# Optimization experiments

Measured on AMD Instinct MI355X. Metric: run time of the kernel, lower is better.

The kernel has to match this reference:

```python
import jax, jax.numpy as jnp
import numpy as np

H = 8
BLEN = 256
NEG = -1e9

def _mask2d(blen, h=32, win=6):
    # precomputed 2D-local mask for tail blocks: query pos in [blen, 2blen),
    # key pos in [0, 2blen); causal + Chebyshev-ish window on a width-h image grid
    cp = np.arange(blen, 2 * blen)[:, None]
    op = np.arange(2 * blen)[None, :]
    causal = op <= cp
    ch, cw = cp // h, cp % h
    oh, ow = op // h, op % h
    ok = causal & (np.abs(ch - oh) <= win) & (np.abs(cw - ow) <= win)
    return np.where(ok, 0.0, NEG).astype(np.float32)

def _causal_mask(blen):
    return np.where(np.tril(np.ones((blen, blen), bool)), 0.0, NEG).astype(np.float32)

def _attn(X, Wq, Wk, Wv, Wo):
    B, L, D = X.shape
    dh = D // H
    split = lambda Y: Y.reshape(B, L, H, dh).transpose(0, 2, 1, 3)  # [B,H,L,dh]
    q = split(X @ Wq) * (dh ** -0.5)
    k = split(X @ Wk)
    v = split(X @ Wv)
    pad = (-L) % BLEN
    if pad:
        q, k, v = (jnp.pad(t, ((0, 0), (0, 0), (0, pad), (0, 0))) for t in (q, k, v))
    Lp = L + pad
    n = Lp // BLEN
    bias1 = jnp.asarray(_causal_mask(BLEN))
    logits1 = jnp.einsum('bhqd,bhkd->bhqk', q[:, :, :BLEN], k[:, :, :BLEN]) + bias1
    first = jax.nn.softmax(logits1, axis=-1) @ v[:, :, :BLEN]  # [B,H,BLEN,dh]
    if n > 1:
        qb = q.reshape(B, H, n, BLEN, dh)
        kb = k.reshape(B, H, n, BLEN, dh)
        vb = v.reshape(B, H, n, BLEN, dh)
        local_k = jnp.concatenate([kb[:, :, :-1], kb[:, :, 1:]], axis=3)  # [B,H,n-1,2B,dh]
        local_v = jnp.concatenate([vb[:, :, :-1], vb[:, :, 1:]], axis=3)
        bias2 = jnp.asarray(_mask2d(BLEN))
        logits2 = jnp.einsum('bhnqd,bhnkd->bhnqk', qb[:, :, 1:], local_k) + bias2
        tail = jnp.einsum('bhnqk,bhnkd->bhnqd', jax.nn.softmax(logits2, axis=-1), local_v)
        tail = tail.reshape(B, H, (n - 1) * BLEN, dh)
        res = jnp.concatenate([first, tail], axis=2)[:, :, :L]
    else:
        res = first[:, :, :L]
    res = res.transpose(0, 2, 1, 3).reshape(B, L, D)
    return res @ Wo

def _ln(x, g, b, eps=1e-6):
    m = x.mean(-1, keepdims=True)
    v = ((x - m) ** 2).mean(-1, keepdims=True)
    return (x - m) / jnp.sqrt(v + eps) * g + b

def setup_inputs() -> dict:
    key = jax.random.key(0)
    ks = jax.random.split(key, 8)
    D, F = 256, 512
    s = 0.02
    return {
        'X': jax.random.normal(ks[0], (32, 1024, D), jnp.float32),
        'Wq': jax.random.normal(ks[1], (D, D), jnp.float32) * s,
        'Wk': jax.random.normal(ks[2], (D, D), jnp.float32) * s,
        'Wv': jax.random.normal(ks[3], (D, D), jnp.float32) * s,
        'Wo': jax.random.normal(ks[4], (D, D), jnp.float32) * s,
        'ln1_g': jnp.ones((D,), jnp.float32),
        'ln1_b': jnp.zeros((D,), jnp.float32),
        'W1': jax.random.normal(ks[5], (D, F), jnp.float32) * s,
        'b1': jnp.zeros((F,), jnp.float32),
        'W2': jax.random.normal(ks[6], (F, D), jnp.float32) * s,
        'b2': jnp.zeros((D,), jnp.float32),
        'ln2_g': jnp.ones((D,), jnp.float32),
        'ln2_b': jnp.zeros((D,), jnp.float32),
    }

def reference(X, Wq, Wk, Wv, Wo, ln1_g, ln1_b, W1, b1, W2, b2, ln2_g, ln2_b):
    y = _attn(X, Wq, Wk, Wv, Wo)
    X = _ln(y + X, ln1_g, ln1_b)
    y = jax.nn.relu(X @ W1 + b1) @ W2 + b2
    return _ln(y + X, ln2_g, ln2_b)
```

## Files before the change

kernel.cpp:

```cpp
#include <hip/hip_runtime.h>

typedef unsigned short u16;
typedef __attribute__((ext_vector_type(8))) short bh8;
typedef __attribute__((ext_vector_type(4))) short s4;
typedef __attribute__((ext_vector_type(4))) short bh4;
typedef __attribute__((ext_vector_type(4))) float fx4;

__device__ __forceinline__ u16 f2b(float f) {
  union { float f; unsigned u; } v; v.f = f;
  unsigned r = v.u + 0x7fffu + ((v.u >> 16) & 1u);
  return (u16)(r >> 16);
}
__device__ __forceinline__ float b2f(u16 h) {
  union { unsigned u; float f; } v; v.u = ((unsigned)h) << 16; return v.f;
}

__device__ __forceinline__ float ex2(float x) {
#if __has_builtin(__builtin_amdgcn_exp2f)
  return __builtin_amdgcn_exp2f(x);
#else
  return __expf(x * 0.6931471805599453f);
#endif
}

__device__ __forceinline__ unsigned cvtpk(float lo, float hi) {
  unsigned r;
  asm("v_cvt_pk_bf16_f32 %0, %1, %2" : "=v"(r) : "v"(lo), "v"(hi));
  return r;
}

#if __has_builtin(__builtin_amdgcn_mfma_f32_16x16x16bf16_1k)
__device__ __forceinline__ fx4 pv_mfma(s4 a, s4 b, fx4 c) {
  return __builtin_amdgcn_mfma_f32_16x16x16bf16_1k(a, b, c, 0, 0, 0);
}
#else
__device__ __forceinline__ fx4 pv_mfma(s4 a, s4 b, fx4 c) {
  asm("v_mfma_f32_16x16x16_bf16 %0, %1, %2, %0" : "+v"(c) : "v"(a), "v"(b));
  return c;
}
#endif

__global__ __launch_bounds__(256) void conv_w_k(const float* __restrict__ Wq, const float* __restrict__ Wk,
                         const float* __restrict__ Wv, const float* __restrict__ Wo,
                         const float* __restrict__ W1, const float* __restrict__ W2,
                         u16* __restrict__ WqkvT, u16* __restrict__ WoT,
                         u16* __restrict__ W1T, u16* __restrict__ W2T) {
  int i = blockIdx.x * 256 + threadIdx.x;
  if (i < 196608) {
    int n = i >> 8, k = i & 255; float v;
    if (n < 256) v = Wq[k*256+n] * 0.25503487359f;
    else if (n < 512) v = Wk[k*256+(n-256)];
    else v = Wv[k*256+(n-512)];
    WqkvT[i] = f2b(v);
  } else if (i < 262144) {
    int j = i - 196608; int n = j >> 8, k = j & 255;
    WoT[j] = f2b(Wo[k*256+n]);
  } else if (i < 393216) {
    int j = i - 262144; int n = j >> 8, k = j & 255;
    W1T[j] = f2b(W1[k*512+n]);
  } else {
    int j = i - 393216; int n = j >> 9, k = j & 511;
    W2T[j] = f2b(W2[k*256+n]);
  }
}

template<int K, int N, int EPI, int AF32>
__global__ __launch_bounds__(256) void gemm_k(
    const void* __restrict__ Av, const u16* __restrict__ BT,
    u16* __restrict__ C0, u16* __restrict__ C1, u16* __restrict__ C2,
    const float* __restrict__ bias) {
  constexpr int BK = 32;
  __shared__ u16 smem[AF32 ? 24576 : 16384];
  constexpr int ABUF = AF32 ? 8192 : 4096;
  constexpr int BOFF = AF32 ? 16384 : 8192;
  const int nx = gridDim.x;
  const int lid = blockIdx.y * nx + blockIdx.x;
  const int xcd = lid & 7;
  const int jj2 = lid >> 3;
  const int m0 = (xcd * (gridDim.y >> 3) + jj2 / nx) * 128;
  const int n0 = (jj2 % nx) * 128;
  const int tid = threadIdx.x, lane = tid & 63, wv = tid >> 6;
  const int wr = wv >> 1, wc = wv & 1, lg = lane >> 4, ll = lane & 15;
  const u16* A16 = (const u16*)Av;
  const float* A32 = (const float*)Av;

  fx4 acc[4][4] = {};

  auto stageB = [&](int buf, int ks) {
#pragma unroll
    for (int i = 0; i < 2; ++i) {
      int c = i*256 + tid;
      int row = c >> 2, ko = (c & 3) * 8;
      const u16* gpB = BT + (size_t)(n0+row)*K + ks + ko;
      int lbase = BOFF + buf*4096 + (i*256 + wv*64) * 8;
      __builtin_amdgcn_global_load_lds((const __attribute__((address_space(1))) void*)gpB,
          (__attribute__((address_space(3))) void*)&smem[lbase], 16, 0, 0);
    }
  };
  auto stageA16 = [&](int buf, int ks) {
#pragma unroll
    for (int i = 0; i < 2; ++i) {
      int c = i*256 + tid;
      int row = c >> 2, ko = (c & 3) * 8;
      const u16* gpA = A16 + (size_t)(m0+row)*K + ks + ko;
      int lbase = buf*ABUF + (i*256 + wv*64) * 8;
      __builtin_amdgcn_global_load_lds((const __attribute__((address_space(1))) void*)gpA,
          (__attribute__((address_space(3))) void*)&smem[lbase], 16, 0, 0);
    }
  };
  auto stageA32 = [&](int buf, int ks) {
#pragma unroll
    for (int i = 0; i < 4; ++i) {
      int c = i*256 + tid;
      int r = c >> 3;
      int po = (c & 7) * 16;
      int lo = po ^ ((r & 7) << 4);
      const float* gpA = A32 + (size_t)(m0 + r)*K + ks + (lo >> 2);
      int lbase = buf*ABUF + (i*256 + wv*64) * 8;
      __builtin_amdgcn_global_load_lds((const __attribute__((address_space(1))) void*)gpA,
          (__attribute__((address_space(3))) void*)&smem[lbase], 16, 0, 0);
    }
  };

  constexpr int NT = K / BK;
  if constexpr (AF32) stageA32(0, 0); else stageA16(0, 0);
  stageB(0, 0);
  __syncthreads();
  int cur = 0;
  for (int t = 0; t < NT; ++t) {
    if (t + 1 < NT) {
      if constexpr (AF32) stageA32(cur ^ 1, (t+1)*BK); else stageA16(cur ^ 1, (t+1)*BK);
      stageB(cur ^ 1, (t+1)*BK);
    }
    bh8 af[4], bfr[4];
    if constexpr (AF32) {
#pragma unroll
      for (int mi = 0; mi < 4; ++mi) {
        int r = wr*64 + mi*16 + ll;
        int sw = (r & 7) << 4;
        int b0 = r*128 + ((lg*32) ^ sw);
        int b1 = r*128 + ((lg*32 + 16) ^ sw);
        float4 a0 = *(const float4*)&smem[cur*ABUF + (b0 >> 1)];
        float4 a1 = *(const float4*)&smem[cur*ABUF + (b1 >> 1)];
        union { unsigned u[4]; bh8 v; } cvt;
        cvt.u[0] = cvtpk(a0.x, a0.y); cvt.u[1] = cvtpk(a0.z, a0.w);
        cvt.u[2] = cvtpk(a1.x, a1.y); cvt.u[3] = cvtpk(a1.z, a1.w);
        af[mi] = cvt.v;
      }
    } else {
#pragma unroll
      for (int mi = 0; mi < 4; ++mi)
        af[mi] = *(const bh8*)&smem[cur*ABUF + (wr*64 + mi*16 + ll)*BK + lg*8];
    }
#pragma unroll
    for (int ni = 0; ni < 4; ++ni)
      bfr[ni] = *(const bh8*)&smem[BOFF + cur*4096 + (wc*64 + ni*16 + ll)*BK + lg*8];
#pragma unroll
    for (int mi = 0; mi < 4; ++mi)
#pragma unroll
      for (int ni = 0; ni < 4; ++ni)
        acc[mi][ni] = __builtin_amdgcn_mfma_f32_16x16x32_bf16(af[mi], bfr[ni], acc[mi][ni], 0, 0, 0);
    __syncthreads();
    cur ^= 1;
  }

  auto swz = [](int r) { return ((r & 14) << 2) ^ ((r & 3) << 5); };
  const bool vt = (EPI == 0) && (n0 >= 512);

  if (!vt) {
    float bv[4];
    if constexpr (EPI >= 2) {
#pragma unroll
      for (int ni = 0; ni < 4; ++ni) bv[ni] = bias[n0 + wc*64 + ni*16 + ll];
    }
#pragma unroll
    for (int mi = 0; mi < 4; ++mi)
#pragma unroll
      for (int ni = 0; ni < 4; ++ni) {
        fx4 v = acc[mi][ni];
        int n = wc*64 + ni*16 + ll;
#pragma unroll
        for (int ii = 0; ii < 2; ++ii) {
          float x0 = v[2*ii], x1 = v[2*ii+1];
          if constexpr (EPI == 2) { x0 = fmaxf(x0 + bv[ni], 0.f); x1 = fmaxf(x1 + bv[ni], 0.f); }
          unsigned pk = cvtpk(x0, x1);
          int mA = wr*64 + mi*16 + lg*4 + 2*ii;
          int mB = mA + 1;
          smem[mA*128 + (n ^ swz(mA))] = (u16)pk;
          smem[mB*128 + (n ^ swz(mB))] = (u16)(pk >> 16);
        }
      }
  } else {
#pragma unroll
    for (int mi = 0; mi < 4; ++mi)
#pragma unroll
      for (int ni = 0; ni < 4; ++ni) {
        fx4 v = acc[mi][ni];
        int n = wc*64 + ni*16 + ll;
        int mb = wr*64 + mi*16 + lg*4;
        uint2 pk;
        pk.x = cvtpk(v[0], v[1]);
        pk.y = cvtpk(v[2], v[3]);
        *(uint2*)&smem[n*128 + (mb ^ swz(n))] = pk;
      }
  }
  __syncthreads();

#pragma unroll
  for (int j = 0; j < 8; ++j) {
    int cid = tid + 256*j;
    int row = cid >> 4, c8 = (cid & 15) << 3;
    bh8 val = *(const bh8*)&smem[row*128 + (c8 ^ swz(row))];
    if constexpr (EPI == 0) {
      if (!vt) {
        int m = m0 + row; int b = m >> 10, l = m & 1023;
        int n = n0 + c8; int hh = (n >> 5) & 7, d = n & 31;
        size_t bh_ = (size_t)(b*8 + hh);
        u16* dst = (n0 < 256) ? C0 : C1;
        *(bh8*)&dst[(bh_*1024 + l)*32 + d] = val;
      } else {
        int n = n0 + row; int hh = (n >> 5) & 7, d = n & 31;
        int m = m0 + c8; int b = m >> 10, l = m & 1023;
        size_t bh_ = (size_t)(b*8 + hh);
        *(bh8*)&C2[(bh_*32 + d)*1024 + l] = val;
      }
    } else {
      *(bh8*)&C0[(size_t)(m0+row)*N + n0 + c8] = val;
    }
  }
}

template<int K, int RF32, int OF32, int BIAS>
__global__ __launch_bounds__(256) void gemm_ln_k(
    const u16* __restrict__ A, const u16* __restrict__ BT,
    const void* __restrict__ resid, const float* __restrict__ bias,
    const float* __restrict__ g, const float* __restrict__ b,
    void* __restrict__ out) {
  constexpr int BK = 32;
  __shared__ u16 smem[20480];
  const int lid = blockIdx.y;
  const int xcd = lid & 7;
  const int jj2 = lid >> 3;
  const int m0 = (xcd * (gridDim.y >> 3) + jj2) * 64;
  const int tid = threadIdx.x, lane = tid & 63, wv = tid >> 6;
  const int wr = wv >> 1, wc = wv & 1, lg = lane >> 4, ll = lane & 15;

  fx4 acc[2][8] = {};

  auto stage = [&](int buf, int ks) {
    {
      int c = tid;
      int row = c >> 2, ko = (c & 3) * 8;
      const u16* gpA = A + (size_t)(m0+row)*K + ks + ko;
      int lbase = wv*512;
      __builtin_amdgcn_global_load_lds((const __attribute__((address_space(1))) void*)gpA,
          (__attribute__((address_space(3))) void*)&smem[buf*2048 + lbase], 16, 0, 0);
    }
#pragma unroll
    for (int i = 0; i < 4; ++i) {
      int c = i*256 + tid;
      int row = c >> 2, ko = (c & 3) * 8;
      const u16* gpB = BT + (size_t)row*K + ks + ko;
      int lbase = (i*256 + wv*64) * 8;
      __builtin_amdgcn_global_load_lds((const __attribute__((address_space(1))) void*)gpB,
          (__attribute__((address_space(3))) void*)&smem[4096 + buf*8192 + lbase], 16, 0, 0);
    }
  };

  constexpr int NT = K / BK;
  stage(0, 0);
  __syncthreads();
  int cur = 0;
  for (int t = 0; t < NT; ++t) {
    if (t + 1 < NT) stage(cur ^ 1, (t+1)*BK);
    bh8 af[2], bfr[8];
#pragma unroll
    for (int mi = 0; mi < 2; ++mi)
      af[mi] = *(const bh8*)&smem[cur*2048 + (wr*32 + mi*16 + ll)*BK + lg*8];
#pragma unroll
    for (int ni = 0; ni < 8; ++ni)
      bfr[ni] = *(const bh8*)&smem[4096 + cur*8192 + (wc*128 + ni*16 + ll)*BK + lg*8];
#pragma unroll
    for (int mi = 0; mi < 2; ++mi)
#pragma unroll
      for (int ni = 0; ni < 8; ++ni)
        acc[mi][ni] = __builtin_amdgcn_mfma_f32_16x16x32_bf16(bfr[ni], af[mi], acc[mi][ni], 0, 0, 0);
    __syncthreads();
    cur ^= 1;
  }

#pragma unroll
  for (int mi = 0; mi < 2; ++mi) {
    int m_l = wr*32 + mi*16 + ll;
    int sx = (m_l & 7) << 1;
#pragma unroll
    for (int ni = 0; ni < 8; ++ni) {
      fx4 v = acc[mi][ni];
      int gidx = (wc*32 + ni*4 + lg) ^ sx;
      uint2 pk;
      pk.x = cvtpk(v[0], v[1]);
      pk.y = cvtpk(v[2], v[3]);
      *(uint2*)&smem[m_l*256 + gidx*4] = pk;
    }
  }
  __syncthreads();

  const int c0 = lane * 4;
  float4 gv = *(const float4*)&g[c0];
  float4 bv = *(const float4*)&b[c0];
  float4 biasv = {0.f, 0.f, 0.f, 0.f};
  if constexpr (BIAS) biasv = *(const float4*)&bias[c0];
#pragma unroll 4
  for (int rr = 0; rr < 16; ++rr) {
    int r = wv*16 + rr;
    bh4 yv = *(const bh4*)&smem[r*256 + ((lane ^ ((r & 7) << 1)) << 2)];
    size_t gbase = (size_t)(m0 + r) * 256 + c0;
    float s0, s1, s2, s3;
    if constexpr (RF32) {
      float4 xv = *(const float4*)&((const float*)resid)[gbase];
      s0 = b2f((u16)yv[0]) + biasv.x + xv.x;
      s1 = b2f((u16)yv[1]) + biasv.y + xv.y;
      s2 = b2f((u16)yv[2]) + biasv.z + xv.z;
      s3 = b2f((u16)yv[3]) + biasv.w + xv.w;
    } else {
      bh4 xv = *(const bh4*)&((const u16*)resid)[gbase];
      s0 = b2f((u16)yv[0]) + biasv.x + b2f((u16)xv[0]);
      s1 = b2f((u16)yv[1]) + biasv.y + b2f((u16)xv[1]);
      s2 = b2f((u16)yv[2]) + biasv.z + b2f((u16)xv[2]);
      s3 = b2f((u16)yv[3]) + biasv.w + b2f((u16)xv[3]);
    }
    float sum = s0 + s1 + s2 + s3;
    float sq  = s0*s0 + s1*s1 + s2*s2 + s3*s3;
#pragma unroll
    for (int msk = 1; msk <= 32; msk <<= 1) {
      sum += __shfl_xor(sum, msk);
      sq  += __shfl_xor(sq, msk);
    }
    float mean = sum * 0.00390625f;
    float var  = sq  * 0.00390625f - mean*mean;
    float rs = rsqrtf(var + 1e-6f);
    float o0 = (s0 - mean)*rs*gv.x + bv.x;
    float o1 = (s1 - mean)*rs*gv.y + bv.y;
    float o2 = (s2 - mean)*rs*gv.z + bv.z;
    float o3 = (s3 - mean)*rs*gv.w + bv.w;
    if constexpr (OF32) {
      float4 o = {o0, o1, o2, o3};
      *(float4*)&((float*)out)[gbase] = o;
    } else {
      bh4 o;
      o[0] = (short)f2b(o0); o[1] = (short)f2b(o1);
      o[2] = (short)f2b(o2); o[3] = (short)f2b(o3);
      *(bh4*)&((u16*)out)[gbase] = o;
    }
  }
}

__global__ __launch_bounds__(256) void attn_k(
    const u16* __restrict__ qw, const u16* __restrict__ kw,
    const u16* __restrict__ vtw, u16* __restrict__ ao) {
  const int qb = blockIdx.x, hh = blockIdx.y, b = blockIdx.z;
  const int tid = threadIdx.x, lane = tid & 63, wv = tid >> 6;
  const int lg = lane >> 4, ll = lane & 15;
  const int kstart = qb ? (qb - 1) * 256 : 0;
  const size_t bh_ = (size_t)(b*8 + hh);
  const u16* kg = kw  + (bh_*1024 + kstart)*32;
  const u16* vg = vtw + bh_*32*1024 + kstart;
  const u16* qg = qw  + (bh_*1024 + qb*256)*32;

  bh8 qf[4];
#pragma unroll
  for (int qi = 0; qi < 4; ++qi)
    qf[qi] = *(const bh8*)&qg[(size_t)(wv*64 + qi*16 + ll)*32 + lg*8];

  fx4 oacc[4][2] = {};
  float lsum[4] = {0.f, 0.f, 0.f, 0.f};
  const fx4 zero = {0.f, 0.f, 0.f, 0.f};

  const int ch0 = wv*2;
  const int lo_w = qb ? ch0 + 2 : 0;
  const int hi_w = qb ? ch0 + 9 : ch0 + 1;

  for (int ohm = lo_w; ohm <= hi_w; ++ohm) {
    const int kb = ohm * 32;
    bh8 kf0 = *(const bh8*)&kg[(size_t)(kb + ll)*32 + lg*8];
    bh8 kf1 = *(const bh8*)&kg[(size_t)(kb + 16 + ll)*32 + lg*8];
    s4 vb[2][2];
#pragma unroll
    for (int cs = 0; cs < 2; ++cs)
#pragma unroll
      for (int dsub = 0; dsub < 2; ++dsub)
        vb[cs][dsub] = *(const s4*)&vg[(size_t)(dsub*16 + ll)*1024 + kb + cs*16 + lg*4];

#pragma unroll
    for (int qi = 0; qi < 4; ++qi) {
      const int ch = ch0 + (qi >> 1);
      const int dlo = qb ? ch + 2 : 0;
      const int dhi = qb ? ch + 8 : ch;
      if (ohm < dlo || ohm > dhi) continue;
      const bool diag = (ohm == dhi);

      fx4 s0 = __builtin_amdgcn_mfma_f32_16x16x32_bf16(kf0, qf[qi], zero, 0, 0, 0);
      fx4 s1 = __builtin_amdgcn_mfma_f32_16x16x32_bf16(kf1, qf[qi], zero, 0, 0, 0);

      const int cw = ll + ((qi & 1) << 4);
      float p[2][4];
      if (!qb && !diag) {
#pragma unroll
        for (int i = 0; i < 4; ++i) { p[0][i] = ex2(s0[i]); p[1][i] = ex2(s1[i]); }
      } else {
        const int off = (qb && !diag) ? 6 : 0;
        const unsigned thr = diag ? (qb ? 7u : 32u) : 13u;
#pragma unroll
        for (int cs = 0; cs < 2; ++cs) {
          const int tb = cw + off - cs*16 - lg*4;
          fx4 sv = cs ? s1 : s0;
#pragma unroll
          for (int i = 0; i < 4; ++i) {
            bool ok = (unsigned)(tb - i) < thr;
            p[cs][i] = ok ? ex2(sv[i]) : 0.f;
          }
        }
      }
      lsum[qi] += (p[0][0]+p[0][1]+p[0][2]+p[0][3]) + (p[1][0]+p[1][1]+p[1][2]+p[1][3]);

#pragma unroll
      for (int cs = 0; cs < 2; ++cs) {
        union { unsigned u[2]; s4 s; } cv;
        cv.u[0] = cvtpk(p[cs][0], p[cs][1]);
        cv.u[1] = cvtpk(p[cs][2], p[cs][3]);
#pragma unroll
        for (int dsub = 0; dsub < 2; ++dsub)
          oacc[qi][dsub] = pv_mfma(cv.s, vb[cs][dsub], oacc[qi][dsub]);
      }
    }
  }

  float rinv[4];
#pragma unroll
  for (int qi = 0; qi < 4; ++qi) {
    float v = lsum[qi];
    v += __shfl_xor(v, 16);
    v += __shfl_xor(v, 32);
    rinv[qi] = 1.0f / v;
  }

  u16* aop = ao + ((size_t)(b*1024 + qb*256))*256 + hh*32;
#pragma unroll
  for (int qi = 0; qi < 4; ++qi) {
    float rq[4];
#pragma unroll
    for (int i = 0; i < 4; ++i) rq[i] = __shfl(rinv[qi], lg*4 + i);
#pragma unroll
    for (int dsub = 0; dsub < 2; ++dsub)
#pragma unroll
      for (int i = 0; i < 4; ++i) {
        int q = wv*64 + qi*16 + lg*4 + i;
        aop[(size_t)q*256 + dsub*16 + ll] = f2b(oacc[qi][dsub][i] * rq[i]);
      }
  }
}

extern "C" void kernel_launch(void* const* d_in, const int* in_sizes, int n_in,
                              void* d_out, int out_size, void* d_ws, size_t ws_size,
                              hipStream_t stream) {
  const float* X    = (const float*)d_in[0];
  const float* Wq   = (const float*)d_in[1];
  const float* Wk   = (const float*)d_in[2];
  const float* Wv   = (const float*)d_in[3];
  const float* Wo   = (const float*)d_in[4];
  const float* ln1g = (const float*)d_in[5];
  const float* ln1b = (const float*)d_in[6];
  const float* W1   = (const float*)d_in[7];
  const float* b1   = (const float*)d_in[8];
  const float* W2   = (const float*)d_in[9];
  const float* b2   = (const float*)d_in[10];
  const float* ln2g = (const float*)d_in[11];
  const float* ln2b = (const float*)d_in[12];
  float* out = (float*)d_out;

  char* ws = (char*)d_ws;
  const size_t A = 32768ull * 256 * 2;
  u16* qws = (u16*)(ws + A);
  u16* kws = (u16*)(ws + 2*A);
  u16* vtw = (u16*)(ws + 3*A);
  u16* ao  = (u16*)(ws);
  u16* x1b = kws;
  u16* hw  = (u16*)(ws);
  u16* WqkvT = (u16*)(ws + 4*A);
  u16* WoT = WqkvT + 196608;
  u16* W1T = WoT + 65536;
  u16* W2T = W1T + 131072;

  conv_w_k<<<2048, 256, 0, stream>>>(Wq, Wk, Wv, Wo, W1, W2, WqkvT, WoT, W1T, W2T);
  gemm_k<256, 768, 0, 1><<<dim3(6, 256), 256, 0, stream>>>(X, WqkvT, qws, kws, vtw, nullptr);
  attn_k<<<dim3(4, 8, 32), 256, 0, stream>>>(qws, kws, vtw, ao);
  gemm_ln_k<256, 1, 0, 0><<<dim3(1, 512), 256, 0, stream>>>(ao, WoT, X, nullptr, ln1g, ln1b, x1b);
  gemm_k<256, 512, 2, 0><<<dim3(4, 256), 256, 0, stream>>>(x1b, W1T, hw, nullptr, nullptr, b1);
  gemm_ln_k<512, 0, 1, 1><<<dim3(1, 512), 256, 0, stream>>>(hw, W2T, x1b, b2, ln2g, ln2b, out);
}
```

Baseline: 119.6 us.

## Triple-buffer GEMM LDS staging with explicit vmcnt waits and raw barriers

```diff
diff --git a/kernel.cpp b/kernel.cpp
--- a/kernel.cpp
+++ b/kernel.cpp
@@ -39,6 +39,12 @@
   return c;
 }
 #endif
+
+#define SBAR() do { \
+  __builtin_amdgcn_sched_barrier(0); \
+  __builtin_amdgcn_s_barrier(); \
+  __builtin_amdgcn_sched_barrier(0); \
+} while (0)
 
 __global__ __launch_bounds__(256) void conv_w_k(const float* __restrict__ Wq, const float* __restrict__ Wk,
                          const float* __restrict__ Wv, const float* __restrict__ Wo,
@@ -70,9 +76,11 @@
     u16* __restrict__ C0, u16* __restrict__ C1, u16* __restrict__ C2,
     const float* __restrict__ bias) {
   constexpr int BK = 32;
-  __shared__ u16 smem[AF32 ? 24576 : 16384];
   constexpr int ABUF = AF32 ? 8192 : 4096;
-  constexpr int BOFF = AF32 ? 16384 : 8192;
+  constexpr int BBUF = 4096;
+  constexpr int BOFF = 3 * ABUF;
+  constexpr int LPI  = AF32 ? 6 : 4;
+  __shared__ u16 smem[3*ABUF + 3*BBUF];
   const int nx = gridDim.x;
   const int lid = blockIdx.y * nx + blockIdx.x;
   const int xcd = lid & 7;
@@ -92,7 +100,7 @@
       int c = i*256 + tid;
       int row = c >> 2, ko = (c & 3) * 8;
       const u16* gpB = BT + (size_t)(n0+row)*K + ks + ko;
-      int lbase = BOFF + buf*4096 + (i*256 + wv*64) * 8;
+      int lbase = BOFF + buf*BBUF + (i*256 + wv*64) * 8;
       __builtin_amdgcn_global_load_lds((const __attribute__((address_space(1))) void*)gpB,
           (__attribute__((address_space(3))) void*)&smem[lbase], 16, 0, 0);
     }
@@ -121,17 +129,26 @@
           (__attribute__((address_space(3))) void*)&smem[lbase], 16, 0, 0);
     }
   };
+  auto stageAB = [&](int buf, int ks) {
+    if constexpr (AF32) stageA32(buf, ks); else stageA16(buf, ks);
+    stageB(buf, ks);
+  };
 
   constexpr int NT = K / BK;
-  if constexpr (AF32) stageA32(0, 0); else stageA16(0, 0);
-  stageB(0, 0);
-  __syncthreads();
+  stageAB(0, 0);
+  stageAB(1, BK);
   int cur = 0;
   for (int t = 0; t < NT; ++t) {
-    if (t + 1 < NT) {
-      if constexpr (AF32) stageA32(cur ^ 1, (t+1)*BK); else stageA16(cur ^ 1, (t+1)*BK);
-      stageB(cur ^ 1, (t+1)*BK);
-    }
+    if (t + 2 < NT) {
+      int nb = cur + 2; if (nb >= 3) nb -= 3;
+      stageAB(nb, (t+2)*BK);
+      asm volatile("s_waitcnt vmcnt(%0)" :: "i"(2*LPI) : "memory");
+    } else if (t + 1 < NT) {
+      asm volatile("s_waitcnt vmcnt(%0)" :: "i"(LPI) : "memory");
+    } else {
+      asm volatile("s_waitcnt vmcnt(0)" ::: "memory");
+    }
+    SBAR();
     bh8 af[4], bfr[4];
     if constexpr (AF32) {
 #pragma unroll
@@ -154,14 +171,14 @@
     }
 #pragma unroll
     for (int ni = 0; ni < 4; ++ni)
-      bfr[ni] = *(const bh8*)&smem[BOFF + cur*4096 + (wc*64 + ni*16 + ll)*BK + lg*8];
+      bfr[ni] = *(const bh8*)&smem[BOFF + cur*BBUF + (wc*64 + ni*16 + ll)*BK + lg*8];
 #pragma unroll
     for (int mi = 0; mi < 4; ++mi)
 #pragma unroll
       for (int ni = 0; ni < 4; ++ni)
         acc[mi][ni] = __builtin_amdgcn_mfma_f32_16x16x32_bf16(af[mi], bfr[ni], acc[mi][ni], 0, 0, 0);
-    __syncthreads();
-    cur ^= 1;
+    SBAR();
+    cur = (cur + 1 == 3) ? 0 : cur + 1;
   }
 
   auto swz = [](int r) { return ((r & 14) << 2) ^ ((r & 3) << 5); };
@@ -237,7 +254,11 @@
     const float* __restrict__ g, const float* __restrict__ b,
     void* __restrict__ out) {
   constexpr int BK = 32;
-  __shared__ u16 smem[20480];
+  constexpr int ABUF = 2048;
+  constexpr int BBUF = 8192;
+  constexpr int BOFF = 3 * ABUF;
+  constexpr int LPI  = 5;
+  __shared__ u16 smem[3*ABUF + 3*BBUF];
   const int lid = blockIdx.y;
   const int xcd = lid & 7;
   const int jj2 = lid >> 3;
@@ -252,41 +273,50 @@
       int c = tid;
       int row = c >> 2, ko = (c & 3) * 8;
       const u16* gpA = A + (size_t)(m0+row)*K + ks + ko;
-      int lbase = wv*512;
+      int lbase = buf*ABUF + wv*512;
       __builtin_amdgcn_global_load_lds((const __attribute__((address_space(1))) void*)gpA,
-          (__attribute__((address_space(3))) void*)&smem[buf*2048 + lbase], 16, 0, 0);
+          (__attribute__((address_space(3))) void*)&smem[lbase], 16, 0, 0);
     }
 #pragma unroll
     for (int i = 0; i < 4; ++i) {
       int c = i*256 + tid;
       int row = c >> 2, ko = (c & 3) * 8;
       const u16* gpB = BT + (size_t)row*K + ks + ko;
-      int lbase = (i*256 + wv*64) * 8;
+      int lbase = BOFF + buf*BBUF + (i*256 + wv*64) * 8;
       __builtin_amdgcn_global_load_lds((const __attribute__((address_space(1))) void*)gpB,
-          (__attribute__((address_space(3))) void*)&smem[4096 + buf*8192 + lbase], 16, 0, 0);
+          (__attribute__((address_space(3))) void*)&smem[lbase], 16, 0, 0);
     }
   };
 
   constexpr int NT = K / BK;
   stage(0, 0);
-  __syncthreads();
+  stage(1, BK);
   int cur = 0;
   for (int t = 0; t < NT; ++t) {
-    if (t + 1 < NT) stage(cur ^ 1, (t+1)*BK);
+    if (t + 2 < NT) {
+      int nb = cur + 2; if (nb >= 3) nb -= 3;
+      stage(nb, (t+2)*BK);
+      asm volatile("s_waitcnt vmcnt(%0)" :: "i"(2*LPI) : "memory");
+    } else if (t + 1 < NT) {
+      asm volatile("s_waitcnt vmcnt(%0)" :: "i"(LPI) : "memory");
+    } else {
+      asm volatile("s_waitcnt vmcnt(0)" ::: "memory");
+    }
+    SBAR();
     bh8 af[2], bfr[8];
 #pragma unroll
     for (int mi = 0; mi < 2; ++mi)
-      af[mi] = *(const bh8*)&smem[cur*2048 + (wr*32 + mi*16 + ll)*BK + lg*8];
+      af[mi] = *(const bh8*)&smem[cur*ABUF + (wr*32 + mi*16 + ll)*BK + lg*8];
 #pragma unroll
     for (int ni = 0; ni < 8; ++ni)
-      bfr[ni] = *(const bh8*)&smem[4096 + cur*8192 + (wc*128 + ni*16 + ll)*BK + lg*8];
+      bfr[ni] = *(const bh8*)&smem[BOFF + cur*BBUF + (wc*128 + ni*16 + ll)*BK + lg*8];
 #pragma unroll
     for (int mi = 0; mi < 2; ++mi)
 #pragma unroll
       for (int ni = 0; ni < 8; ++ni)
         acc[mi][ni] = __builtin_amdgcn_mfma_f32_16x16x32_bf16(bfr[ni], af[mi], acc[mi][ni], 0, 0, 0);
-    __syncthreads();
-    cur ^= 1;
+    SBAR();
+    cur = (cur + 1 == 3) ? 0 : cur + 1;
   }
 
 #pragma unroll
```

New measurement: 128.1 us. 1.07x slower.

## Enlarge gemm_k tile to 256x128 with 512-thread blocks sharing B tiles

Applied to the files above, without the earlier changes.

```diff
diff --git a/kernel.cpp b/kernel.cpp
--- a/kernel.cpp
+++ b/kernel.cpp
@@ -65,19 +65,20 @@
 }
 
 template<int K, int N, int EPI, int AF32>
-__global__ __launch_bounds__(256) void gemm_k(
+__global__ __launch_bounds__(512) void gemm_k(
     const void* __restrict__ Av, const u16* __restrict__ BT,
     u16* __restrict__ C0, u16* __restrict__ C1, u16* __restrict__ C2,
     const float* __restrict__ bias) {
   constexpr int BK = 32;
-  __shared__ u16 smem[AF32 ? 24576 : 16384];
-  constexpr int ABUF = AF32 ? 8192 : 4096;
-  constexpr int BOFF = AF32 ? 16384 : 8192;
+  constexpr int ABUF = AF32 ? 16384 : 8192;
+  constexpr int BBUF = 4096;
+  constexpr int BOFF = 2 * ABUF;
+  __shared__ u16 smem[2*ABUF + 2*BBUF];
   const int nx = gridDim.x;
   const int lid = blockIdx.y * nx + blockIdx.x;
   const int xcd = lid & 7;
   const int jj2 = lid >> 3;
-  const int m0 = (xcd * (gridDim.y >> 3) + jj2 / nx) * 128;
+  const int m0 = (xcd * (gridDim.y >> 3) + jj2 / nx) * 256;
   const int n0 = (jj2 % nx) * 128;
   const int tid = threadIdx.x, lane = tid & 63, wv = tid >> 6;
   const int wr = wv >> 1, wc = wv & 1, lg = lane >> 4, ll = lane & 15;
@@ -87,23 +88,20 @@
   fx4 acc[4][4] = {};
 
   auto stageB = [&](int buf, int ks) {
-#pragma unroll
-    for (int i = 0; i < 2; ++i) {
-      int c = i*256 + tid;
-      int row = c >> 2, ko = (c & 3) * 8;
-      const u16* gpB = BT + (size_t)(n0+row)*K + ks + ko;
-      int lbase = BOFF + buf*4096 + (i*256 + wv*64) * 8;
-      __builtin_amdgcn_global_load_lds((const __attribute__((address_space(1))) void*)gpB,
-          (__attribute__((address_space(3))) void*)&smem[lbase], 16, 0, 0);
-    }
+    int c = tid;
+    int row = c >> 2, ko = (c & 3) * 8;
+    const u16* gpB = BT + (size_t)(n0+row)*K + ks + ko;
+    int lbase = BOFF + buf*BBUF + wv*64*8;
+    __builtin_amdgcn_global_load_lds((const __attribute__((address_space(1))) void*)gpB,
+        (__attribute__((address_space(3))) void*)&smem[lbase], 16, 0, 0);
   };
   auto stageA16 = [&](int buf, int ks) {
 #pragma unroll
     for (int i = 0; i < 2; ++i) {
-      int c = i*256 + tid;
+      int c = i*512 + tid;
       int row = c >> 2, ko = (c & 3) * 8;
       const u16* gpA = A16 + (size_t)(m0+row)*K + ks + ko;
-      int lbase = buf*ABUF + (i*256 + wv*64) * 8;
+      int lbase = buf*ABUF + (i*512 + wv*64) * 8;
       __builtin_amdgcn_global_load_lds((const __attribute__((address_space(1))) void*)gpA,
           (__attribute__((address_space(3))) void*)&smem[lbase], 16, 0, 0);
     }
@@ -111,27 +109,27 @@
   auto stageA32 = [&](int buf, int ks) {
 #pragma unroll
     for (int i = 0; i < 4; ++i) {
-      int c = i*256 + tid;
+      int c = i*512 + tid;
       int r = c >> 3;
       int po = (c & 7) * 16;
       int lo = po ^ ((r & 7) << 4);
       const float* gpA = A32 + (size_t)(m0 + r)*K + ks + (lo >> 2);
-      int lbase = buf*ABUF + (i*256 + wv*64) * 8;
+      int lbase = buf*ABUF + (i*512 + wv*64) * 8;
       __builtin_amdgcn_global_load_lds((const __attribute__((address_space(1))) void*)gpA,
           (__attribute__((address_space(3))) void*)&smem[lbase], 16, 0, 0);
     }
   };
+  auto stageAB = [&](int buf, int ks) {
+    if constexpr (AF32) stageA32(buf, ks); else stageA16(buf, ks);
+    stageB(buf, ks);
+  };
 
   constexpr int NT = K / BK;
-  if constexpr (AF32) stageA32(0, 0); else stageA16(0, 0);
-  stageB(0, 0);
+  stageAB(0, 0);
   __syncthreads();
   int cur = 0;
   for (int t = 0; t < NT; ++t) {
-    if (t + 1 < NT) {
-      if constexpr (AF32) stageA32(cur ^ 1, (t+1)*BK); else stageA16(cur ^ 1, (t+1)*BK);
-      stageB(cur ^ 1, (t+1)*BK);
-    }
+    if (t + 1 < NT) stageAB(cur ^ 1, (t+1)*BK);
     bh8 af[4], bfr[4];
     if constexpr (AF32) {
 #pragma unroll
@@ -154,7 +152,7 @@
     }
 #pragma unroll
     for (int ni = 0; ni < 4; ++ni)
-      bfr[ni] = *(const bh8*)&smem[BOFF + cur*4096 + (wc*64 + ni*16 + ll)*BK + lg*8];
+      bfr[ni] = *(const bh8*)&smem[BOFF + cur*BBUF + (wc*64 + ni*16 + ll)*BK + lg*8];
 #pragma unroll
     for (int mi = 0; mi < 4; ++mi)
 #pragma unroll
@@ -167,65 +165,76 @@
   auto swz = [](int r) { return ((r & 14) << 2) ^ ((r & 3) << 5); };
   const bool vt = (EPI == 0) && (n0 >= 512);
 
-  if (!vt) {
-    float bv[4];
-    if constexpr (EPI >= 2) {
-#pragma unroll
-      for (int ni = 0; ni < 4; ++ni) bv[ni] = bias[n0 + wc*64 + ni*16 + ll];
-    }
-#pragma unroll
-    for (int mi = 0; mi < 4; ++mi)
-#pragma unroll
-      for (int ni = 0; ni < 4; ++ni) {
-        fx4 v = acc[mi][ni];
-        int n = wc*64 + ni*16 + ll;
-#pragma unroll
-        for (int ii = 0; ii < 2; ++ii) {
-          float x0 = v[2*ii], x1 = v[2*ii+1];
-          if constexpr (EPI == 2) { x0 = fmaxf(x0 + bv[ni], 0.f); x1 = fmaxf(x1 + bv[ni], 0.f); }
-          unsigned pk = cvtpk(x0, x1);
-          int mA = wr*64 + mi*16 + lg*4 + 2*ii;
-          int mB = mA + 1;
-          smem[mA*128 + (n ^ swz(mA))] = (u16)pk;
-          smem[mB*128 + (n ^ swz(mB))] = (u16)(pk >> 16);
+  float bv[4];
+  if constexpr (EPI >= 2) {
+#pragma unroll
+    for (int ni = 0; ni < 4; ++ni) bv[ni] = bias[n0 + wc*64 + ni*16 + ll];
+  }
+
+#pragma unroll
+  for (int half = 0; half < 2; ++half) {
+    if (half) __syncthreads();
+    if ((wr >> 1) == half) {
+      const int lwr = wr & 1;
+      if (!vt) {
+#pragma unroll
+        for (int mi = 0; mi < 4; ++mi)
+#pragma unroll
+          for (int ni = 0; ni < 4; ++ni) {
+            fx4 v = acc[mi][ni];
+            int n = wc*64 + ni*16 + ll;
+#pragma unroll
+            for (int ii = 0; ii < 2; ++ii) {
+              float x0 = v[2*ii], x1 = v[2*ii+1];
+              if constexpr (EPI == 2) { x0 = fmaxf(x0 + bv[ni], 0.f); x1 = fmaxf(x1 + bv[ni], 0.f); }
+              unsigned pk = cvtpk(x0, x1);
+              int mA = lwr*64 + mi*16 + lg*4 + 2*ii;
+              int mB = mA + 1;
+              smem[mA*128 + (n ^ swz(mA))] = (u16)pk;
+              smem[mB*128 + (n ^ swz(mB))] = (u16)(pk >> 16);
+            }
+          }
+      } else {
+#pragma unroll
+        for (int mi = 0; mi < 4; ++mi)
+#pragma unroll
+          for (int ni = 0; ni < 4; ++ni) {
+            fx4 v = acc[mi][ni];
+            int n = wc*64 + ni*16 + ll;
+            int mb = lwr*64 + mi*16 + lg*4;
+            uint2 pk;
+            pk.x = cvtpk(v[0], v[1]);
+            pk.y = cvtpk(v[2], v[3]);
+            *(uint2*)&smem[n*128 + (mb ^ ((n & 7) << 3))] = pk;
+          }
+      }
+    }
+    __syncthreads();
+
+#pragma unroll
+    for (int j = 0; j < 4; ++j) {
+      int cid = tid + 512*j;
+      int row = cid >> 4, c8 = (cid & 15) << 3;
+      if constexpr (EPI == 0) {
+        if (!vt) {
+          bh8 val = *(const bh8*)&smem[row*128 + (c8 ^ swz(row))];
+          int m = m0 + half*128 + row; int b = m >> 10, l = m & 1023;
+          int n = n0 + c8; int hh = (n >> 5) & 7, d = n & 31;
+          size_t bh_ = (size_t)(b*8 + hh);
+          u16* dst = (n0 < 256) ? C0 : C1;
+          *(bh8*)&dst[(bh_*1024 + l)*32 + d] = val;
+        } else {
+          bh8 val = *(const bh8*)&smem[row*128 + (c8 ^ ((row & 7) << 3))];
+          int n = n0 + row; int hh = (n >> 5) & 7, d = n & 31;
+          int m = m0 + half*128 + c8; int b = m >> 10, l = m & 1023;
+          size_t bh_ = (size_t)(b*8 + hh);
+          *(bh8*)&C2[(bh_*32 + d)*1024 + l] = val;
         }
+      } else {
+        bh8 val = *(const bh8*)&smem[row*128 + (c8 ^ swz(row))];
+        int m = m0 + half*128 + row;
+        *(bh8*)&C0[(size_t)m*N + n0 + c8] = val;
       }
-  } else {
-#pragma unroll
-    for (int mi = 0; mi < 4; ++mi)
-#pragma unroll
-      for (int ni = 0; ni < 4; ++ni) {
-        fx4 v = acc[mi][ni];
-        int n = wc*64 + ni*16 + ll;
-        int mb = wr*64 + mi*16 + lg*4;
-        uint2 pk;
-        pk.x = cvtpk(v[0], v[1]);
-        pk.y = cvtpk(v[2], v[3]);
-        *(uint2*)&smem[n*128 + (mb ^ swz(n))] = pk;
-      }
-  }
-  __syncthreads();
-
-#pragma unroll
-  for (int j = 0; j < 8; ++j) {
-    int cid = tid + 256*j;
-    int row = cid >> 4, c8 = (cid & 15) << 3;
-    bh8 val = *(const bh8*)&smem[row*128 + (c8 ^ swz(row))];
-    if constexpr (EPI == 0) {
-      if (!vt) {
-        int m = m0 + row; int b = m >> 10, l = m & 1023;
-        int n = n0 + c8; int hh = (n >> 5) & 7, d = n & 31;
-        size_t bh_ = (size_t)(b*8 + hh);
-        u16* dst = (n0 < 256) ? C0 : C1;
-        *(bh8*)&dst[(bh_*1024 + l)*32 + d] = val;
-      } else {
-        int n = n0 + row; int hh = (n >> 5) & 7, d = n & 31;
-        int m = m0 + c8; int b = m >> 10, l = m & 1023;
-        size_t bh_ = (size_t)(b*8 + hh);
-        *(bh8*)&C2[(bh_*32 + d)*1024 + l] = val;
-      }
-    } else {
-      *(bh8*)&C0[(size_t)(m0+row)*N + n0 + c8] = val;
     }
   }
 }
@@ -492,9 +501,9 @@
   u16* W2T = W1T + 131072;
 
   conv_w_k<<<2048, 256, 0, stream>>>(Wq, Wk, Wv, Wo, W1, W2, WqkvT, WoT, W1T, W2T);
-  gemm_k<256, 768, 0, 1><<<dim3(6, 256), 256, 0, stream>>>(X, WqkvT, qws, kws, vtw, nullptr);
+  gemm_k<256, 768, 0, 1><<<dim3(6, 128), 512, 0, stream>>>(X, WqkvT, qws, kws, vtw, nullptr);
   attn_k<<<dim3(4, 8, 32), 256, 0, stream>>>(qws, kws, vtw, ao);
   gemm_ln_k<256, 1, 0, 0><<<dim3(1, 512), 256, 0, stream>>>(ao, WoT, X, nullptr, ln1g, ln1b, x1b);
-  gemm_k<256, 512, 2, 0><<<dim3(4, 256), 256, 0, stream>>>(x1b, W1T, hw, nullptr, nullptr, b1);
+  gemm_k<256, 512, 2, 0><<<dim3(4, 128), 512, 0, stream>>>(x1b, W1T, hw, nullptr, nullptr, b1);
   gemm_ln_k<512, 0, 1, 1><<<dim3(1, 512), 256, 0, stream>>>(hw, W2T, x1b, b2, ln2g, ln2b, out);
 }
```

Result: slower. 132.0 us (+10.4%).

## Add dedicated QKV projection kernel with full-K weight tile in LDS

Applied to the files above, without the earlier changes.

```diff
diff --git a/kernel.cpp b/kernel.cpp
--- a/kernel.cpp
+++ b/kernel.cpp
@@ -64,15 +64,124 @@
   }
 }
 
+__global__ __launch_bounds__(256) void qkv_k(
+    const float* __restrict__ X, const u16* __restrict__ BT,
+    u16* __restrict__ qw, u16* __restrict__ kw, u16* __restrict__ vtw) {
+  __shared__ u16 smem[16384];
+  constexpr int nx = 12;
+  const int lid = blockIdx.y * nx + blockIdx.x;
+  const int xcd = lid & 7;
+  const int jj2 = lid >> 3;
+  const int m0 = (xcd * (gridDim.y >> 3) + jj2 / nx) * 256;
+  const int n0 = (jj2 % nx) * 64;
+  const int tid = threadIdx.x, lane = tid & 63, wv = tid >> 6;
+  const int lg = lane >> 4, ll = lane & 15;
+
+#pragma unroll
+  for (int i = 0; i < 8; ++i) {
+    int c = i*256 + tid;
+    int row = c >> 5, kc = c & 31;
+    const u16* gp = BT + (size_t)(n0+row)*256 + ((kc ^ (row & 7)) << 3);
+    int lbase = (i*256 + wv*64) * 8;
+    __builtin_amdgcn_global_load_lds((const __attribute__((address_space(1))) void*)gp,
+        (__attribute__((address_space(3))) void*)&smem[lbase], 16, 0, 0);
+  }
+  __syncthreads();
+
+  fx4 acc[4][4] = {};
+  const float* aw = X + (size_t)(m0 + wv*64)*256;
+
+#pragma unroll
+  for (int t = 0; t < 8; ++t) {
+    bh8 af[4], bfr[4];
+#pragma unroll
+    for (int mi = 0; mi < 4; ++mi) {
+      const float* ap = aw + (size_t)(mi*16 + ll)*256 + t*32 + lg*8;
+      float4 a0 = *(const float4*)ap;
+      float4 a1 = *(const float4*)(ap + 4);
+      union { unsigned u[4]; bh8 v; } cvt;
+      cvt.u[0] = cvtpk(a0.x, a0.y); cvt.u[1] = cvtpk(a0.z, a0.w);
+      cvt.u[2] = cvtpk(a1.x, a1.y); cvt.u[3] = cvtpk(a1.z, a1.w);
+      af[mi] = cvt.v;
+    }
+#pragma unroll
+    for (int ni = 0; ni < 4; ++ni) {
+      int row = ni*16 + ll;
+      bfr[ni] = *(const bh8*)&smem[row*256 + (((t*4 + lg) ^ (ll & 7)) << 3)];
+    }
+#pragma unroll
+    for (int mi = 0; mi < 4; ++mi)
+#pragma unroll
+      for (int ni = 0; ni < 4; ++ni)
+        acc[mi][ni] = __builtin_amdgcn_mfma_f32_16x16x32_bf16(af[mi], bfr[ni], acc[mi][ni], 0, 0, 0);
+  }
+
+  __syncthreads();
+  const bool vt = (n0 >= 512);
+
+  if (!vt) {
+#pragma unroll
+    for (int mi = 0; mi < 4; ++mi)
+#pragma unroll
+      for (int ni = 0; ni < 4; ++ni) {
+        fx4 v = acc[mi][ni];
+        int n = ni*16 + ll;
+#pragma unroll
+        for (int ii = 0; ii < 2; ++ii) {
+          unsigned pk = cvtpk(v[2*ii], v[2*ii+1]);
+          int mA = wv*64 + mi*16 + lg*4 + 2*ii;
+          int mB = mA + 1;
+          smem[mA*64 + (n ^ ((mA & 7) << 3))] = (u16)pk;
+          smem[mB*64 + (n ^ ((mB & 7) << 3))] = (u16)(pk >> 16);
+        }
+      }
+  } else {
+#pragma unroll
+    for (int mi = 0; mi < 4; ++mi)
+#pragma unroll
+      for (int ni = 0; ni < 4; ++ni) {
+        fx4 v = acc[mi][ni];
+        int n = ni*16 + ll;
+        int mb = wv*64 + mi*16 + lg*4;
+        uint2 pk;
+        pk.x = cvtpk(v[0], v[1]);
+        pk.y = cvtpk(v[2], v[3]);
+        *(uint2*)&smem[n*256 + (mb ^ ((n & 7) << 3))] = pk;
+      }
+  }
+  __syncthreads();
+
+#pragma unroll
+  for (int j = 0; j < 8; ++j) {
+    int cid = tid + 256*j;
+    if (!vt) {
+      int row = cid >> 3, g = cid & 7;
+      bh8 val = *(const bh8*)&smem[row*64 + ((g*8) ^ ((row & 7) << 3))];
+      int m = m0 + row; int b = m >> 10, l = m & 1023;
+      int n = n0 + g*8; int hh = (n >> 5) & 7, d = n & 31;
+      size_t bh_ = (size_t)(b*8 + hh);
+      u16* dst = (n0 < 256) ? qw : kw;
+      *(bh8*)&dst[(bh_*1024 + l)*32 + d] = val;
+    } else {
+      int row = cid >> 5, mc = cid & 31;
+      bh8 val = *(const bh8*)&smem[row*256 + ((mc*8) ^ ((row & 7) << 3))];
+      int n = n0 + row; int hh = (n >> 5) & 7, d = n & 31;
+      int m = m0 + mc*8; int b = m >> 10, l = m & 1023;
+      size_t bh_ = (size_t)(b*8 + hh);
+      *(bh8*)&vtw[(bh_*32 + d)*1024 + l] = val;
+    }
+  }
+}
+
 template<int K, int N, int EPI, int AF32>
 __global__ __launch_bounds__(256) void gemm_k(
     const void* __restrict__ Av, const u16* __restrict__ BT,
     u16* __restrict__ C0, u16* __restrict__ C1, u16* __restrict__ C2,
     const float* __restrict__ bias) {
   constexpr int BK = 32;
-  __shared__ u16 smem[AF32 ? 24576 : 16384];
   constexpr int ABUF = AF32 ? 8192 : 4096;
   constexpr int BOFF = AF32 ? 16384 : 8192;
+  __shared__ u16 smem[AF32 ? 24576 : 16384];
   const int nx = gridDim.x;
   const int lid = blockIdx.y * nx + blockIdx.x;
   const int xcd = lid & 7;
@@ -165,9 +274,8 @@
   }
 
   auto swz = [](int r) { return ((r & 14) << 2) ^ ((r & 3) << 5); };
-  const bool vt = (EPI == 0) && (n0 >= 512);
-
-  if (!vt) {
+
+  {
     float bv[4];
     if constexpr (EPI >= 2) {
 #pragma unroll
@@ -190,19 +298,6 @@
           smem[mB*128 + (n ^ swz(mB))] = (u16)(pk >> 16);
         }
       }
-  } else {
-#pragma unroll
-    for (int mi = 0; mi < 4; ++mi)
-#pragma unroll
-      for (int ni = 0; ni < 4; ++ni) {
-        fx4 v = acc[mi][ni];
-        int n = wc*64 + ni*16 + ll;
-        int mb = wr*64 + mi*16 + lg*4;
-        uint2 pk;
-        pk.x = cvtpk(v[0], v[1]);
-        pk.y = cvtpk(v[2], v[3]);
-        *(uint2*)&smem[n*128 + (mb ^ swz(n))] = pk;
-      }
   }
   __syncthreads();
 
@@ -211,22 +306,7 @@
     int cid = tid + 256*j;
     int row = cid >> 4, c8 = (cid & 15) << 3;
     bh8 val = *(const bh8*)&smem[row*128 + (c8 ^ swz(row))];
-    if constexpr (EPI == 0) {
-      if (!vt) {
-        int m = m0 + row; int b = m >> 10, l = m & 1023;
-        int n = n0 + c8; int hh = (n >> 5) & 7, d = n & 31;
-        size_t bh_ = (size_t)(b*8 + hh);
-        u16* dst = (n0 < 256) ? C0 : C1;
-        *(bh8*)&dst[(bh_*1024 + l)*32 + d] = val;
-      } else {
-        int n = n0 + row; int hh = (n >> 5) & 7, d = n & 31;
-        int m = m0 + c8; int b = m >> 10, l = m & 1023;
-        size_t bh_ = (size_t)(b*8 + hh);
-        *(bh8*)&C2[(bh_*32 + d)*1024 + l] = val;
-      }
-    } else {
-      *(bh8*)&C0[(size_t)(m0+row)*N + n0 + c8] = val;
-    }
+    *(bh8*)&C0[(size_t)(m0+row)*N + n0 + c8] = val;
   }
 }
 
@@ -492,7 +572,7 @@
   u16* W2T = W1T + 131072;
 
   conv_w_k<<<2048, 256, 0, stream>>>(Wq, Wk, Wv, Wo, W1, W2, WqkvT, WoT, W1T, W2T);
-  gemm_k<256, 768, 0, 1><<<dim3(6, 256), 256, 0, stream>>>(X, WqkvT, qws, kws, vtw, nullptr);
+  qkv_k<<<dim3(12, 128), 256, 0, stream>>>(X, WqkvT, qws, kws, vtw);
   attn_k<<<dim3(4, 8, 32), 256, 0, stream>>>(qws, kws, vtw, ao);
   gemm_ln_k<256, 1, 0, 0><<<dim3(1, 512), 256, 0, stream>>>(ao, WoT, X, nullptr, ln1g, ln1b, x1b);
   gemm_k<256, 512, 2, 0><<<dim3(4, 256), 256, 0, stream>>>(x1b, W1T, hw, nullptr, nullptr, b1);
```

Result: slower. 154.3 us (+29.1%).
